# Performance work log

Measured on AMD Instinct MI355X. Metric: run time of the kernel, lower is better.

The kernel has to match this reference:

```python
import jax, jax.numpy as jnp
import numpy as np

VOCAB = 256
D = 512
M = 4            # max_block_size
DS = 2           # downsample_rate
K = 5            # conv kernel size
B = 8
L = 8192


def setup_inputs() -> dict:
    key = jax.random.key(0)
    k1, k2, k3, k4, k5 = jax.random.split(key, 5)
    input_ids = jax.random.randint(k1, (B, L), 0, VOCAB)
    emb = jax.random.normal(k2, (VOCAB, D), dtype=jnp.float32) * 0.02
    emb = emb.at[0].set(0.0)  # padding_idx=0
    conv_w = jax.random.normal(k3, (D, D, K), dtype=jnp.float32) * (1.0 / np.sqrt(D * K))
    conv_b = jax.random.normal(k4, (D,), dtype=jnp.float32) * 0.01
    score_w = jax.random.normal(k5, (D,), dtype=jnp.float32) * (1.0 / np.sqrt(D))
    return {"input_ids": input_ids, "emb": emb, "conv_w": conv_w,
            "conv_b": conv_b, "score_w": score_w}


def _gbst(input_ids, emb, conv_w, conv_b, score_w):
    x = emb[input_ids]                                  # [B, L, D]
    # pre-conv (same padding), NCH layout
    xc = jnp.transpose(x, (0, 2, 1))                    # [B, D, L]
    xc = jax.lax.conv_general_dilated(
        xc, conv_w, window_strides=(1,), padding=[((K - 1) // 2, (K - 1) // 2)],
        dimension_numbers=("NCH", "OIH", "NCH"))
    x = jnp.transpose(xc, (0, 2, 1)) + conv_b           # [B, L, D]

    Lx = x.shape[1]
    cands, scores = [], []
    for b in range(1, M + 1):
        pad = (b - Lx % b) % b
        xp = jnp.pad(x, ((0, 0), (0, pad), (0, 0))) if pad else x
        pooled = xp.reshape(B, -1, b, x.shape[-1]).mean(axis=2)   # [B, Lx/b, D]
        s = pooled @ score_w                                       # [B, Lx/b]
        up = jnp.repeat(pooled, b, axis=1)[:, :Lx]                 # [B, Lx, D]
        us = jnp.repeat(s, b, axis=1)[:, :Lx]                      # [B, Lx]
        cands.append(up)
        scores.append(us)
    candidates = jnp.stack(cands, axis=-1)              # [B, L, D, M]
    block_scores = jax.nn.softmax(jnp.stack(scores, axis=-1), axis=-1)  # [B, L, M]
    latent = jnp.einsum("bldm,blm->bld", candidates, block_scores)      # [B, L, D]

    # final downsample mean-pool
    Ll = latent.shape[1]
    pad = (DS - Ll % DS) % DS
    if pad:
        latent = jnp.pad(latent, ((0, 0), (0, pad), (0, 0)))
    latent = latent.reshape(B, -1, DS, latent.shape[-1]).mean(axis=2)
    return latent                                        # [B, L//DS, D]


def reference(input_ids, emb, conv_w, conv_b, score_w):
    return _gbst(input_ids, emb, conv_w, conv_b, score_w)
```

## Files before the change

kernel.cpp:

```cpp
#include <hip/hip_runtime.h>

#define VOCABN 256
#define DN 512
#define DSN 2
#define KN 5
#define BN 8
#define LN 8192
#define WN 12
#define NW12 ((LN + WN - 1) / WN)
#define LOUTN (LN / DSN)
#define NROWS (KN * VOCABN)
#define ROWB (DN * 2)
#define KPLANE (VOCABN * ROWB)
#define ZOFFB (NROWS * ROWB)
#define SBIAS_IDX (NROWS + 4 * VOCABN + 1)
#define ISP 4

#define GP_BYTES (ISP * NROWS * DN * 4)
#define G_OFF GP_BYTES
#define SW_OFF (G_OFF + 2305 * ROWB)

typedef float nf2 __attribute__((ext_vector_type(2)));

__device__ inline unsigned short f2bf(float f) {
  unsigned int x = __float_as_uint(f);
  return (unsigned short)((x + 0x7FFFu + ((x >> 16) & 1u)) >> 16);
}

__global__ __launch_bounds__(256) void gbuild_kernel(const float* __restrict__ emb,
                                                     const float* __restrict__ cw,
                                                     float* __restrict__ Gp) {
  const int bx = blockIdx.x;
  const int vt = bx & 3, ot = (bx >> 2) & 7;
  const int kq = bx >> 5;
  const int k = kq % 5, isp = kq / 5;
  const int v0 = vt * 64, o0 = ot * 64;
  const int tid = threadIdx.x;
  const int ox = tid & 15, vx = tid >> 4;
  const int c = tid & 31, rr = tid >> 5;
  __shared__ float se[32][68];
  __shared__ float wt[32][68];
  float acc[4][4] = {};
  for (int ic = 0; ic < 4; ++ic) {
    const int i0 = isp * 128 + ic * 32;
    __syncthreads();
#pragma unroll
    for (int p = 0; p < 8; ++p) {
      const int q = p * 8 + rr;
      se[c][q] = emb[(size_t)(v0 + q) * DN + i0 + c];
      wt[c][q] = cw[((size_t)(o0 + q) * DN + i0 + c) * KN + k];
    }
    __syncthreads();
#pragma unroll
    for (int i = 0; i < 32; ++i) {
      const float4 a = *(const float4*)&se[i][vx * 4];
      const float4 b = *(const float4*)&wt[i][ox * 4];
      acc[0][0] += a.x * b.x; acc[0][1] += a.x * b.y; acc[0][2] += a.x * b.z; acc[0][3] += a.x * b.w;
      acc[1][0] += a.y * b.x; acc[1][1] += a.y * b.y; acc[1][2] += a.y * b.z; acc[1][3] += a.y * b.w;
      acc[2][0] += a.z * b.x; acc[2][1] += a.z * b.y; acc[2][2] += a.z * b.z; acc[2][3] += a.z * b.w;
      acc[3][0] += a.w * b.x; acc[3][1] += a.w * b.y; acc[3][2] += a.w * b.z; acc[3][3] += a.w * b.w;
    }
  }
#pragma unroll
  for (int vi = 0; vi < 4; ++vi) {
    const int row = k * VOCABN + v0 + vx * 4 + vi;
    float4 f;
    f.x = acc[vi][0];
    f.y = acc[vi][1];
    f.z = acc[vi][2];
    f.w = acc[vi][3];
    *(float4*)(Gp + ((size_t)isp * NROWS + row) * DN + o0 + ox * 4) = f;
  }
}

__global__ __launch_bounds__(256) void gswr_kernel(const float* __restrict__ Gp,
                                                   const float* __restrict__ conv_b,
                                                   const float* __restrict__ score_w,
                                                   unsigned int* __restrict__ G32,
                                                   float* __restrict__ SW) {
  const int r = blockIdx.x;
  const int tid = threadIdx.x;
  __shared__ float sred[4];
  if (r >= NROWS && r < NROWS + 5) {
    const int z = NROWS + (r - NROWS) * VOCABN;
    G32[(size_t)z * 256 + tid] = 0u;
    if (tid == 0) SW[z] = 0.f;
    return;
  }
  const float2 sw2 = *(const float2*)(score_w + tid * 2);
  float sdot;
  if (r == NROWS + 5) {
    const float2 cb2 = *(const float2*)(conv_b + tid * 2);
    sdot = cb2.x * sw2.x + cb2.y * sw2.y;
  } else {
    float x = 0.f, y = 0.f;
#pragma unroll
    for (int isp = 0; isp < ISP; ++isp) {
      const float2 p = *(const float2*)(Gp + ((size_t)isp * NROWS + r) * DN + tid * 2);
      x += p.x;
      y += p.y;
    }
    G32[(size_t)r * 256 + tid] = (unsigned)f2bf(x) | ((unsigned)f2bf(y) << 16);
    sdot = x * sw2.x + y * sw2.y;
  }
#pragma unroll
  for (int off = 32; off > 0; off >>= 1) sdot += __shfl_xor(sdot, off, 64);
  if ((tid & 63) == 0) sred[tid >> 6] = sdot;
  __syncthreads();
  if (tid == 0) {
    const float v = sred[0] + sred[1] + sred[2] + sred[3];
    if (r == NROWS + 5) SW[SBIAS_IDX] = v;
    else SW[r] = v;
  }
}

__global__ __launch_bounds__(256, 5) void gbst_main_kernel(const int* __restrict__ ids,
                                                           const unsigned short* __restrict__ G,
                                                           const float* __restrict__ SW,
                                                           const float* __restrict__ conv_b,
                                                           float* __restrict__ out) {
  const int blk = blockIdx.x;
  const int b = blk / NW12;
  const int w = blk % NW12;
  const int l0 = w * WN;
  const int tid = threadIdx.x;

  __shared__ float t_s[WN];
  __shared__ float4 wm_s[WN];

  int joff[WN + 4];
#pragma unroll
  for (int j = 0; j < WN + 4; ++j) {
    const int p = l0 + j - 2;
    const bool v = ((unsigned)p < (unsigned)LN);
    const int a = v ? (b * LN + p) : 0;
    const int id = ids[a];
    joff[j] = v ? (id * ROWB) : ZOFFB;
  }

  const char* Gc = (const char*)G;
  float2 y[WN];
#pragma unroll
  for (int s = 0; s < WN; ++s) {
    float ax = 0.f, ay = 0.f;
#pragma unroll
    for (int kk = 0; kk < KN; ++kk) {
      const unsigned g = ((const unsigned*)(Gc + (joff[s + kk] + kk * KPLANE)))[tid];
      ax += __uint_as_float(g << 16);
      ay += __uint_as_float(g & 0xFFFF0000u);
    }
    y[s].x = ax;
    y[s].y = ay;
  }
  const float2 bias = *(const float2*)(conv_b + tid * 2);
#pragma unroll
  for (int s = 0; s < WN; ++s) {
    const bool valid = (l0 + s) < LN;
    y[s].x = valid ? y[s].x + bias.x : 0.f;
    y[s].y = valid ? y[s].y + bias.y : 0.f;
  }

  if (tid < 64) {
    const float sbias = SW[SBIAS_IDX];
    float t[WN];
#pragma unroll
    for (int s = 0; s < WN; ++s) {
      float tv = sbias;
#pragma unroll
      for (int kk = 0; kk < KN; ++kk) tv += SW[(joff[s + kk] >> 10) + kk * VOCABN];
      t[s] = (l0 + s < LN) ? tv : 0.f;
    }
    if (tid == 0) {
#pragma unroll
      for (int s = 0; s < WN; ++s) t_s[s] = t[s];
    }
    if (tid < WN && l0 + tid < LN) {
      const int ll = tid;
      float s1 = t_s[ll];
      int j2 = ll & ~1;
      float s2 = 0.5f * (t_s[j2] + t_s[j2 + 1]);
      int j3 = (ll / 3) * 3;
      float s3 = (1.f / 3.f) * (t_s[j3] + t_s[j3 + 1] + t_s[j3 + 2]);
      int j4 = ll & ~3;
      float s4 = 0.25f * (t_s[j4] + t_s[j4 + 1] + t_s[j4 + 2] + t_s[j4 + 3]);
      float mx = fmaxf(fmaxf(s1, s2), fmaxf(s3, s4));
      float e1 = __expf(s1 - mx), e2 = __expf(s2 - mx);
      float e3 = __expf(s3 - mx), e4 = __expf(s4 - mx);
      float inv = 1.f / (e1 + e2 + e3 + e4);
      wm_s[ll] = make_float4(e1 * inv, e2 * inv, e3 * inv, e4 * inv);
    }
  }

  float2 S2[6], S3[4], S4[3];
#pragma unroll
  for (int j = 0; j < 6; ++j) {
    S2[j].x = y[2 * j].x + y[2 * j + 1].x;
    S2[j].y = y[2 * j].y + y[2 * j + 1].y;
  }
#pragma unroll
  for (int j = 0; j < 4; ++j) {
    S3[j].x = y[3 * j].x + y[3 * j + 1].x + y[3 * j + 2].x;
    S3[j].y = y[3 * j].y + y[3 * j + 1].y + y[3 * j + 2].y;
  }
#pragma unroll
  for (int j = 0; j < 3; ++j) {
    S4[j].x = S2[2 * j].x + S2[2 * j + 1].x;
    S4[j].y = S2[2 * j].y + S2[2 * j + 1].y;
  }
  __syncthreads();

#pragma unroll
  for (int jo = 0; jo < WN / 2; ++jo) {
    const int orow = (l0 >> 1) + jo;
    if (orow < LOUTN) {
      float ax = 0.f, ay = 0.f;
#pragma unroll
      for (int dl = 0; dl < 2; ++dl) {
        const int ll = 2 * jo + dl;
        const float4 wv = wm_s[ll];
        const float c2 = wv.y * 0.5f;
        const float c3 = wv.z * (1.f / 3.f);
        const float c4 = wv.w * 0.25f;
        ax += wv.x * y[ll].x + c2 * S2[jo].x + c3 * S3[ll / 3].x + c4 * S4[jo >> 1].x;
        ay += wv.x * y[ll].y + c2 * S2[jo].y + c3 * S3[ll / 3].y + c4 * S4[jo >> 1].y;
      }
      nf2 o2;
      o2.x = 0.5f * ax;
      o2.y = 0.5f * ay;
      __builtin_nontemporal_store(o2, (nf2*)(out + ((size_t)b * LOUTN + orow) * DN + tid * 2));
    }
  }
}

extern "C" void kernel_launch(void* const* d_in, const int* in_sizes, int n_in,
                              void* d_out, int out_size, void* d_ws, size_t ws_size,
                              hipStream_t stream) {
  const int* ids = (const int*)d_in[0];
  const float* emb = (const float*)d_in[1];
  const float* conv_w = (const float*)d_in[2];
  const float* conv_b = (const float*)d_in[3];
  const float* score_w = (const float*)d_in[4];
  float* out = (float*)d_out;

  char* ws = (char*)d_ws;
  float* Gp = (float*)ws;
  unsigned short* G = (unsigned short*)(ws + G_OFF);
  float* SW = (float*)(ws + SW_OFF);

  gbuild_kernel<<<dim3(640), dim3(256), 0, stream>>>(emb, conv_w, Gp);
  gswr_kernel<<<dim3(NROWS + 6), dim3(256), 0, stream>>>(Gp, conv_b, score_w,
                                                         (unsigned int*)G, SW);
  gbst_main_kernel<<<dim3(BN * NW12), dim3(256), 0, stream>>>(ids, G, SW, conv_b, out);
}
```

Baseline: 49.47 us.

## Restructure G-table build to load conv weights coalesced for all taps at once

The emb×conv_w precompute kernel now processes all five kernel taps in one block, reading conv_w rows with contiguous float4 loads and scattering them into a per-tap shared-memory tile. Before, each tap was handled by a separate block through strided scalar loads. The input-channel split doubles from 4 to 8 and the vocab tile shrinks to 32, so there are 512 blocks with 40 accumulators per thread. The cost is more partial-sum rows for the reduction kernel to read and higher register pressure.

Result: slower. 55.03 us (+11.2%).

```diff
diff --git a/kernel.cpp b/kernel.cpp
--- a/kernel.cpp
+++ b/kernel.cpp
@@ -14,11 +14,11 @@
 #define KPLANE (VOCABN * ROWB)
 #define ZOFFB (NROWS * ROWB)
 #define SBIAS_IDX (NROWS + 4 * VOCABN + 1)
-#define ISP 4
-
-#define GP_BYTES (ISP * NROWS * DN * 4)
+#define ISP 8
+
+#define GP_BYTES ((size_t)ISP * NROWS * DN * 4)
 #define G_OFF GP_BYTES
-#define SW_OFF (G_OFF + 2305 * ROWB)
+#define SW_OFF (G_OFF + (size_t)2305 * ROWB)
 
 typedef float nf2 __attribute__((ext_vector_type(2)));
 
@@ -31,46 +31,64 @@
                                                      const float* __restrict__ cw,
                                                      float* __restrict__ Gp) {
   const int bx = blockIdx.x;
-  const int vt = bx & 3, ot = (bx >> 2) & 7;
-  const int kq = bx >> 5;
-  const int k = kq % 5, isp = kq / 5;
-  const int v0 = vt * 64, o0 = ot * 64;
+  const int vt = bx & 7, ot = (bx >> 3) & 7, isp = bx >> 6;
+  const int v0 = vt * 32, o0 = ot * 64;
   const int tid = threadIdx.x;
   const int ox = tid & 15, vx = tid >> 4;
-  const int c = tid & 31, rr = tid >> 5;
-  __shared__ float se[32][68];
-  __shared__ float wt[32][68];
-  float acc[4][4] = {};
-  for (int ic = 0; ic < 4; ++ic) {
-    const int i0 = isp * 128 + ic * 32;
+
+  __shared__ float se[32][36];
+  __shared__ float wt[KN][32][68];
+
+  float acc[2][4][KN] = {};
+
+  const int ec = tid & 31, eg = tid >> 5;
+  const int co = tid >> 2, cj = tid & 3;
+
+  for (int sub = 0; sub < 2; ++sub) {
+    const int i0 = isp * 64 + sub * 32;
     __syncthreads();
 #pragma unroll
-    for (int p = 0; p < 8; ++p) {
-      const int q = p * 8 + rr;
-      se[c][q] = emb[(size_t)(v0 + q) * DN + i0 + c];
-      wt[c][q] = cw[((size_t)(o0 + q) * DN + i0 + c) * KN + k];
+    for (int p = 0; p < 4; ++p) {
+      const int q = eg * 4 + p;
+      se[ec][q] = emb[(size_t)(v0 + q) * DN + i0 + ec];
+    }
+    const float* crow = cw + (size_t)(o0 + co) * (DN * KN) + (size_t)i0 * KN;
+#pragma unroll
+    for (int it = 0; it < 10; ++it) {
+      const int f4 = cj + it * 4;
+      const float4 w4 = *(const float4*)(crow + f4 * 4);
+      const int e0 = f4 * 4;
+      wt[(e0 + 0) % KN][(e0 + 0) / KN][co] = w4.x;
+      wt[(e0 + 1) % KN][(e0 + 1) / KN][co] = w4.y;
+      wt[(e0 + 2) % KN][(e0 + 2) / KN][co] = w4.z;
+      wt[(e0 + 3) % KN][(e0 + 3) / KN][co] = w4.w;
     }
     __syncthreads();
-#pragma unroll
+#pragma unroll 4
     for (int i = 0; i < 32; ++i) {
-      const float4 a = *(const float4*)&se[i][vx * 4];
-      const float4 b = *(const float4*)&wt[i][ox * 4];
-      acc[0][0] += a.x * b.x; acc[0][1] += a.x * b.y; acc[0][2] += a.x * b.z; acc[0][3] += a.x * b.w;
-      acc[1][0] += a.y * b.x; acc[1][1] += a.y * b.y; acc[1][2] += a.y * b.z; acc[1][3] += a.y * b.w;
-      acc[2][0] += a.z * b.x; acc[2][1] += a.z * b.y; acc[2][2] += a.z * b.z; acc[2][3] += a.z * b.w;
-      acc[3][0] += a.w * b.x; acc[3][1] += a.w * b.y; acc[3][2] += a.w * b.z; acc[3][3] += a.w * b.w;
-    }
-  }
-#pragma unroll
-  for (int vi = 0; vi < 4; ++vi) {
-    const int row = k * VOCABN + v0 + vx * 4 + vi;
-    float4 f;
-    f.x = acc[vi][0];
-    f.y = acc[vi][1];
-    f.z = acc[vi][2];
-    f.w = acc[vi][3];
-    *(float4*)(Gp + ((size_t)isp * NROWS + row) * DN + o0 + ox * 4) = f;
-  }
+      const float2 a = *(const float2*)&se[i][vx * 2];
+#pragma unroll
+      for (int k = 0; k < KN; ++k) {
+        const float4 b = *(const float4*)&wt[k][i][ox * 4];
+        acc[0][0][k] += a.x * b.x; acc[0][1][k] += a.x * b.y;
+        acc[0][2][k] += a.x * b.z; acc[0][3][k] += a.x * b.w;
+        acc[1][0][k] += a.y * b.x; acc[1][1][k] += a.y * b.y;
+        acc[1][2][k] += a.y * b.z; acc[1][3][k] += a.y * b.w;
+      }
+    }
+  }
+#pragma unroll
+  for (int vi = 0; vi < 2; ++vi)
+#pragma unroll
+    for (int k = 0; k < KN; ++k) {
+      const int row = k * VOCABN + v0 + vx * 2 + vi;
+      float4 f;
+      f.x = acc[vi][0][k];
+      f.y = acc[vi][1][k];
+      f.z = acc[vi][2][k];
+      f.w = acc[vi][3][k];
+      *(float4*)(Gp + ((size_t)isp * NROWS + row) * DN + o0 + ox * 4) = f;
+    }
 }
 
 __global__ __launch_bounds__(256) void gswr_kernel(const float* __restrict__ Gp,
@@ -247,7 +265,7 @@
   unsigned short* G = (unsigned short*)(ws + G_OFF);
   float* SW = (float*)(ws + SW_OFF);
 
-  gbuild_kernel<<<dim3(640), dim3(256), 0, stream>>>(emb, conv_w, Gp);
+  gbuild_kernel<<<dim3(512), dim3(256), 0, stream>>>(emb, conv_w, Gp);
   gswr_kernel<<<dim3(NROWS + 6), dim3(256), 0, stream>>>(Gp, conv_b, score_w,
                                                          (unsigned int*)G, SW);
   gbst_main_kernel<<<dim3(BN * NW12), dim3(256), 0, stream>>>(ids, G, SW, conv_b, out);
```

## Map one window per wavefront with 16-byte gathers and no LDS sync

Applied to the files above, without the earlier changes.

The main kernel now gives each 64-lane wavefront its own 12-position window instead of one window per 256-thread block. Each lane covers 8 channels and reads them with 16-byte bf16 gathers. Every lane recomputes the block-score softmax from the scalar-broadcast ids, which removes the shared-memory staging and the block-wide barrier. Token ids are made wave-uniform with readfirstlane. In exchange, each lane holds far more registers (12x8 accumulators), so the occupancy hint drops from 5 to 3, and the output stores become ordinary rather than nontemporal.

Result: slower. 51.71 us (+4.5%).

```diff
diff --git a/kernel.cpp b/kernel.cpp
--- a/kernel.cpp
+++ b/kernel.cpp
@@ -8,6 +8,7 @@
 #define LN 8192
 #define WN 12
 #define NW12 ((LN + WN - 1) / WN)
+#define NWIN (BN * NW12)
 #define LOUTN (LN / DSN)
 #define NROWS (KN * VOCABN)
 #define ROWB (DN * 2)
@@ -16,11 +17,9 @@
 #define SBIAS_IDX (NROWS + 4 * VOCABN + 1)
 #define ISP 4
 
-#define GP_BYTES (ISP * NROWS * DN * 4)
+#define GP_BYTES ((size_t)ISP * NROWS * DN * 4)
 #define G_OFF GP_BYTES
-#define SW_OFF (G_OFF + 2305 * ROWB)
-
-typedef float nf2 __attribute__((ext_vector_type(2)));
+#define SW_OFF (G_OFF + (size_t)2305 * ROWB)
 
 __device__ inline unsigned short f2bf(float f) {
   unsigned int x = __float_as_uint(f);
@@ -114,19 +113,18 @@
   }
 }
 
-__global__ __launch_bounds__(256, 5) void gbst_main_kernel(const int* __restrict__ ids,
+__global__ __launch_bounds__(256, 3) void gbst_main_kernel(const int* __restrict__ ids,
                                                            const unsigned short* __restrict__ G,
                                                            const float* __restrict__ SW,
                                                            const float* __restrict__ conv_b,
                                                            float* __restrict__ out) {
-  const int blk = blockIdx.x;
-  const int b = blk / NW12;
-  const int w = blk % NW12;
+  const int tid = threadIdx.x;
+  const int lane = tid & 63;
+  const int wave = __builtin_amdgcn_readfirstlane(tid >> 6);
+  const int win = blockIdx.x * 4 + wave;
+  const int b = win / NW12;
+  const int w = win - b * NW12;
   const int l0 = w * WN;
-  const int tid = threadIdx.x;
-
-  __shared__ float t_s[WN];
-  __shared__ float4 wm_s[WN];
 
   int joff[WN + 4];
 #pragma unroll
@@ -134,100 +132,87 @@
     const int p = l0 + j - 2;
     const bool v = ((unsigned)p < (unsigned)LN);
     const int a = v ? (b * LN + p) : 0;
-    const int id = ids[a];
+    const int id = __builtin_amdgcn_readfirstlane(ids[a]);
     joff[j] = v ? (id * ROWB) : ZOFFB;
   }
 
-  const char* Gc = (const char*)G;
-  float2 y[WN];
+  const char* Gc = (const char*)G + lane * 16;
+  float y[WN][8];
 #pragma unroll
   for (int s = 0; s < WN; ++s) {
-    float ax = 0.f, ay = 0.f;
+#pragma unroll
+    for (int c = 0; c < 8; ++c) y[s][c] = 0.f;
 #pragma unroll
     for (int kk = 0; kk < KN; ++kk) {
-      const unsigned g = ((const unsigned*)(Gc + (joff[s + kk] + kk * KPLANE)))[tid];
-      ax += __uint_as_float(g << 16);
-      ay += __uint_as_float(g & 0xFFFF0000u);
-    }
-    y[s].x = ax;
-    y[s].y = ay;
-  }
-  const float2 bias = *(const float2*)(conv_b + tid * 2);
+      const uint4 g = *(const uint4*)(Gc + (joff[s + kk] + kk * KPLANE));
+      y[s][0] += __uint_as_float(g.x << 16);
+      y[s][1] += __uint_as_float(g.x & 0xFFFF0000u);
+      y[s][2] += __uint_as_float(g.y << 16);
+      y[s][3] += __uint_as_float(g.y & 0xFFFF0000u);
+      y[s][4] += __uint_as_float(g.z << 16);
+      y[s][5] += __uint_as_float(g.z & 0xFFFF0000u);
+      y[s][6] += __uint_as_float(g.w << 16);
+      y[s][7] += __uint_as_float(g.w & 0xFFFF0000u);
+    }
+  }
+  float bias[8];
+  *(float4*)&bias[0] = *(const float4*)(conv_b + lane * 8);
+  *(float4*)&bias[4] = *(const float4*)(conv_b + lane * 8 + 4);
 #pragma unroll
   for (int s = 0; s < WN; ++s) {
     const bool valid = (l0 + s) < LN;
-    y[s].x = valid ? y[s].x + bias.x : 0.f;
-    y[s].y = valid ? y[s].y + bias.y : 0.f;
-  }
-
-  if (tid < 64) {
-    const float sbias = SW[SBIAS_IDX];
-    float t[WN];
-#pragma unroll
-    for (int s = 0; s < WN; ++s) {
-      float tv = sbias;
-#pragma unroll
-      for (int kk = 0; kk < KN; ++kk) tv += SW[(joff[s + kk] >> 10) + kk * VOCABN];
-      t[s] = (l0 + s < LN) ? tv : 0.f;
-    }
-    if (tid == 0) {
-#pragma unroll
-      for (int s = 0; s < WN; ++s) t_s[s] = t[s];
-    }
-    if (tid < WN && l0 + tid < LN) {
-      const int ll = tid;
-      float s1 = t_s[ll];
-      int j2 = ll & ~1;
-      float s2 = 0.5f * (t_s[j2] + t_s[j2 + 1]);
-      int j3 = (ll / 3) * 3;
-      float s3 = (1.f / 3.f) * (t_s[j3] + t_s[j3 + 1] + t_s[j3 + 2]);
-      int j4 = ll & ~3;
-      float s4 = 0.25f * (t_s[j4] + t_s[j4 + 1] + t_s[j4 + 2] + t_s[j4 + 3]);
-      float mx = fmaxf(fmaxf(s1, s2), fmaxf(s3, s4));
-      float e1 = __expf(s1 - mx), e2 = __expf(s2 - mx);
-      float e3 = __expf(s3 - mx), e4 = __expf(s4 - mx);
-      float inv = 1.f / (e1 + e2 + e3 + e4);
-      wm_s[ll] = make_float4(e1 * inv, e2 * inv, e3 * inv, e4 * inv);
-    }
-  }
-
-  float2 S2[6], S3[4], S4[3];
-#pragma unroll
-  for (int j = 0; j < 6; ++j) {
-    S2[j].x = y[2 * j].x + y[2 * j + 1].x;
-    S2[j].y = y[2 * j].y + y[2 * j + 1].y;
-  }
-#pragma unroll
-  for (int j = 0; j < 4; ++j) {
-    S3[j].x = y[3 * j].x + y[3 * j + 1].x + y[3 * j + 2].x;
-    S3[j].y = y[3 * j].y + y[3 * j + 1].y + y[3 * j + 2].y;
-  }
-#pragma unroll
-  for (int j = 0; j < 3; ++j) {
-    S4[j].x = S2[2 * j].x + S2[2 * j + 1].x;
-    S4[j].y = S2[2 * j].y + S2[2 * j + 1].y;
-  }
-  __syncthreads();
+#pragma unroll
+    for (int c = 0; c < 8; ++c) y[s][c] = valid ? y[s][c] + bias[c] : 0.f;
+  }
+
+  const float sbias = SW[SBIAS_IDX];
+  float t[WN];
+#pragma unroll
+  for (int s = 0; s < WN; ++s) {
+    float tv = sbias;
+#pragma unroll
+    for (int kk = 0; kk < KN; ++kk) tv += SW[(joff[s + kk] >> 10) + kk * VOCABN];
+    t[s] = (l0 + s < LN) ? tv : 0.f;
+  }
 
 #pragma unroll
   for (int jo = 0; jo < WN / 2; ++jo) {
     const int orow = (l0 >> 1) + jo;
     if (orow < LOUTN) {
-      float ax = 0.f, ay = 0.f;
+      float a[8];
+#pragma unroll
+      for (int c = 0; c < 8; ++c) a[c] = 0.f;
 #pragma unroll
       for (int dl = 0; dl < 2; ++dl) {
         const int ll = 2 * jo + dl;
-        const float4 wv = wm_s[ll];
-        const float c2 = wv.y * 0.5f;
-        const float c3 = wv.z * (1.f / 3.f);
-        const float c4 = wv.w * 0.25f;
-        ax += wv.x * y[ll].x + c2 * S2[jo].x + c3 * S3[ll / 3].x + c4 * S4[jo >> 1].x;
-        ay += wv.x * y[ll].y + c2 * S2[jo].y + c3 * S3[ll / 3].y + c4 * S4[jo >> 1].y;
+        const float s1 = t[ll];
+        const int j2 = ll & ~1;
+        const float s2 = 0.5f * (t[j2] + t[j2 + 1]);
+        const int j3 = (ll / 3) * 3;
+        const float s3 = (1.f / 3.f) * (t[j3] + t[j3 + 1] + t[j3 + 2]);
+        const int j4 = ll & ~3;
+        const float s4 = 0.25f * (t[j4] + t[j4 + 1] + t[j4 + 2] + t[j4 + 3]);
+        const float mx = fmaxf(fmaxf(s1, s2), fmaxf(s3, s4));
+        const float e1 = __expf(s1 - mx), e2 = __expf(s2 - mx);
+        const float e3 = __expf(s3 - mx), e4 = __expf(s4 - mx);
+        const float inv = 1.f / (e1 + e2 + e3 + e4);
+        const float c1 = e1 * inv;
+        const float c2 = e2 * inv * 0.5f;
+        const float c3 = e3 * inv * (1.f / 3.f);
+        const float c4 = e4 * inv * 0.25f;
+#pragma unroll
+        for (int c = 0; c < 8; ++c) {
+          a[c] += c1 * y[ll][c] + c2 * (y[j2][c] + y[j2 + 1][c]) +
+                  c3 * (y[j3][c] + y[j3 + 1][c] + y[j3 + 2][c]) +
+                  c4 * (y[j4][c] + y[j4 + 1][c] + y[j4 + 2][c] + y[j4 + 3][c]);
+        }
       }
-      nf2 o2;
-      o2.x = 0.5f * ax;
-      o2.y = 0.5f * ay;
-      __builtin_nontemporal_store(o2, (nf2*)(out + ((size_t)b * LOUTN + orow) * DN + tid * 2));
+      float* orow_p = out + ((size_t)b * LOUTN + orow) * DN + lane * 8;
+      float4 o0, o1;
+      o0.x = 0.5f * a[0]; o0.y = 0.5f * a[1]; o0.z = 0.5f * a[2]; o0.w = 0.5f * a[3];
+      o1.x = 0.5f * a[4]; o1.y = 0.5f * a[5]; o1.z = 0.5f * a[6]; o1.w = 0.5f * a[7];
+      *(float4*)orow_p = o0;
+      *(float4*)(orow_p + 4) = o1;
     }
   }
 }
@@ -250,5 +235,5 @@
   gbuild_kernel<<<dim3(640), dim3(256), 0, stream>>>(emb, conv_w, Gp);
   gswr_kernel<<<dim3(NROWS + 6), dim3(256), 0, stream>>>(Gp, conv_b, score_w,
                                                          (unsigned int*)G, SW);
-  gbst_main_kernel<<<dim3(BN * NW12), dim3(256), 0, stream>>>(ids, G, SW, conv_b, out);
-}
+  gbst_main_kernel<<<dim3(NWIN / 4), dim3(256), 0, stream>>>(ids, G, SW, conv_b, out);
+}
```
